# Kernel tuning notes

Hardware: AMD Instinct MI355X
Metric: run time of the kernel (lower is better)

The kernel has to match this reference:

```python
import jax, jax.numpy as jnp
import numpy as np

NEG_SLOPE = 0.2
# relation r: src node type SRC[r], dst node type DST[r]; 0=Drug, 1=Disease
# order: TREATS, TREATED_BY, HAS_CONTRAIND, CONTRAIND_BY, HAS_PARENTCODE, HAS_CHILDCODE, INTERACTS
SRC = (0, 1, 0, 1, 1, 1, 0)
DST = (1, 0, 1, 0, 1, 1, 0)

N_DRUG, N_DIS, D_IN, HID, OUT, E = 20000, 40000, 256, 128, 128, 150000


def _gat(x_src, x_dst, edge_index, Ws, Wd, a_s, a_d, b):
    # single-head PyG GATConv, add_self_loops=False
    hs = x_src @ Ws                      # [Ns, H]
    hd = x_dst @ Wd                      # [Nd, H]
    src, dst = edge_index[0], edge_index[1]
    n_dst = x_dst.shape[0]
    alpha_src = hs @ a_s                 # [Ns]
    alpha_dst = hd @ a_d                 # [Nd]
    alpha = jax.nn.leaky_relu(alpha_src[src] + alpha_dst[dst], NEG_SLOPE)  # [E]
    amax = jax.ops.segment_max(alpha, dst, num_segments=n_dst)
    amax = jnp.where(jnp.isfinite(amax), amax, 0.0)
    ex = jnp.exp(alpha - amax[dst])
    denom = jax.ops.segment_sum(ex, dst, num_segments=n_dst)
    coef = ex / (denom[dst] + 1e-16)     # per-destination softmax (PyG softmax)
    out = jax.ops.segment_sum(hs[src] * coef[:, None], dst, num_segments=n_dst)
    return out + b


def _hetero_layer(xd, xi, edges, Ws, Wd, a_s, a_d, b):
    feats = (xd, xi)
    H = b.shape[1]
    outs = [jnp.zeros((xd.shape[0], H), xd.dtype), jnp.zeros((xi.shape[0], H), xi.dtype)]
    for r in range(7):
        o = _gat(feats[SRC[r]], feats[DST[r]], edges[r], Ws[r], Wd[r], a_s[r], a_d[r], b[r])
        outs[DST[r]] = outs[DST[r]] + o   # HeteroConv aggr='sum'
    return outs[0], outs[1]


def setup_inputs() -> dict:
    key = jax.random.key(0)
    ks = jax.random.split(key, 32)
    x_drug = jax.random.normal(ks[0], (N_DRUG, D_IN), jnp.float32)
    x_disease = jax.random.normal(ks[1], (N_DIS, D_IN), jnp.float32)
    nsz = (N_DRUG, N_DIS)
    edges = []
    for r in range(7):
        s = jax.random.randint(ks[2 + 2 * r], (E,), 0, nsz[SRC[r]], jnp.int32)
        d = jax.random.randint(ks[3 + 2 * r], (E,), 0, nsz[DST[r]], jnp.int32)
        edges.append(jnp.stack([s, d]))
    s = 0.1
    W1s = s * jax.random.normal(ks[16], (7, D_IN, HID), jnp.float32)
    W1d = s * jax.random.normal(ks[17], (7, D_IN, HID), jnp.float32)
    W1d = W1d.at[6].set(W1s[6])  # INTERACTS shares src/dst lin (GATConv(-1,...))
    a1s = s * jax.random.normal(ks[18], (7, HID), jnp.float32)
    a1d = s * jax.random.normal(ks[19], (7, HID), jnp.float32)
    b1 = jnp.zeros((7, HID), jnp.float32)
    W2s = s * jax.random.normal(ks[20], (7, HID, HID), jnp.float32)
    W2d = s * jax.random.normal(ks[21], (7, HID, HID), jnp.float32)
    W2d = W2d.at[6].set(W2s[6])
    a2s = s * jax.random.normal(ks[22], (7, HID), jnp.float32)
    a2d = s * jax.random.normal(ks[23], (7, HID), jnp.float32)
    b2 = jnp.zeros((7, HID), jnp.float32)
    W_drug = s * jax.random.normal(ks[24], (HID, OUT), jnp.float32)
    b_drug = jnp.zeros((OUT,), jnp.float32)
    W_dis = s * jax.random.normal(ks[25], (HID, OUT), jnp.float32)
    b_dis = jnp.zeros((OUT,), jnp.float32)
    return {"x_drug": x_drug, "x_disease": x_disease,
            "e_treats": edges[0], "e_treated_by": edges[1], "e_contraind": edges[2],
            "e_contraind_by": edges[3], "e_parent": edges[4], "e_child": edges[5],
            "e_interacts": edges[6],
            "W1s": W1s, "W1d": W1d, "a1s": a1s, "a1d": a1d, "b1": b1,
            "W2s": W2s, "W2d": W2d, "a2s": a2s, "a2d": a2d, "b2": b2,
            "W_drug": W_drug, "b_drug": b_drug, "W_dis": W_dis, "b_dis": b_dis}


def reference(x_drug, x_disease, e_treats, e_treated_by, e_contraind, e_contraind_by,
              e_parent, e_child, e_interacts,
              W1s, W1d, a1s, a1d, b1, W2s, W2d, a2s, a2d, b2,
              W_drug, b_drug, W_dis, b_dis):
    edges = (e_treats, e_treated_by, e_contraind, e_contraind_by, e_parent, e_child, e_interacts)
    xd, xi = _hetero_layer(x_drug, x_disease, edges, W1s, W1d, a1s, a1d, b1)
    xd, xi = jax.nn.relu(xd), jax.nn.relu(xi)  # dropout is identity (eval mode)
    xd, xi = _hetero_layer(xd, xi, edges, W2s, W2d, a2s, a2d, b2)
    out_drug = jax.nn.relu(xd @ W_drug + b_drug)
    out_disease = jax.nn.relu(xi @ W_dis + b_dis)
    return out_drug, out_disease
```

## Files before the change

kernel.cpp:

```cpp
#include <hip/hip_runtime.h>
#include <stdint.h>

#define NDRUG 20000
#define NDIS  40000
#define HID   128
#define NE    150000
#define NREL  7
#define RPSTR (NDIS + 1)
#define NS_TOT (NREL * RPSTR)

typedef unsigned short ushort_t;
typedef __attribute__((ext_vector_type(8))) short bf16x8;
typedef __attribute__((ext_vector_type(4))) float f32x4;
typedef const __attribute__((address_space(1))) void gv_t;
typedef __attribute__((address_space(3))) void lv_t;

__device__ __forceinline__ ushort_t f2bf(float f) {
  unsigned u = __float_as_uint(f);
  u += 0x7FFFu + ((u >> 16) & 1u);
  return (ushort_t)(u >> 16);
}
__device__ __forceinline__ float bf2f(ushort_t h) {
  return __uint_as_float(((unsigned)h) << 16);
}

template<bool BIAS, bool RELU, bool BF16OUT>
__global__ __launch_bounds__(256) void mfma_gemm(
    const ushort_t* __restrict__ A, const ushort_t* __restrict__ BT,
    const float* __restrict__ bias, void* __restrict__ Cout, int M, int N, int K)
{
  __shared__ ushort_t As[128 * 32];
  __shared__ ushort_t Bs[128 * 32];
  const int tid = threadIdx.x;
  const int m0 = blockIdx.x * 128;
  const int n0 = blockIdx.y * 128;
  const int wave = tid >> 6, lane = tid & 63;
  const int wm = wave & 1, wn = wave >> 1;
  const int l15 = lane & 15, lk = lane >> 4;

  const int rowS = wave * 16 + (lane >> 2);
  const int chunk = (lane & 3) * 8;
  const int grA0 = min(m0 + rowS, M - 1);
  const int grA1 = min(m0 + rowS + 64, M - 1);
  const int grB0 = n0 + rowS;
  const int grB1 = n0 + rowS + 64;
  const ushort_t* ga0 = A + (size_t)grA0 * K + chunk;
  const ushort_t* ga1 = A + (size_t)grA1 * K + chunk;
  const ushort_t* gb0 = BT + (size_t)grB0 * K + chunk;
  const ushort_t* gb1 = BT + (size_t)grB1 * K + chunk;

  f32x4 acc[4][4] = {};

  for (int k0 = 0; k0 < K; k0 += 32) {
    __syncthreads();
    __builtin_amdgcn_global_load_lds((gv_t*)(ga0 + k0), (lv_t*)(As + wave * 512), 16, 0, 0);
    __builtin_amdgcn_global_load_lds((gv_t*)(ga1 + k0), (lv_t*)(As + wave * 512 + 2048), 16, 0, 0);
    __builtin_amdgcn_global_load_lds((gv_t*)(gb0 + k0), (lv_t*)(Bs + wave * 512), 16, 0, 0);
    __builtin_amdgcn_global_load_lds((gv_t*)(gb1 + k0), (lv_t*)(Bs + wave * 512 + 2048), 16, 0, 0);
    __syncthreads();

    bf16x8 af[4], bfg[4];
    #pragma unroll
    for (int m = 0; m < 4; ++m)
      af[m] = *reinterpret_cast<const bf16x8*>(&As[(wm * 64 + m * 16 + l15) * 32 + lk * 8]);
    #pragma unroll
    for (int n = 0; n < 4; ++n)
      bfg[n] = *reinterpret_cast<const bf16x8*>(&Bs[(wn * 64 + n * 16 + l15) * 32 + lk * 8]);
    #pragma unroll
    for (int m = 0; m < 4; ++m)
      #pragma unroll
      for (int n = 0; n < 4; ++n)
        acc[m][n] = __builtin_amdgcn_mfma_f32_16x16x32_bf16(af[m], bfg[n], acc[m][n], 0, 0, 0);
  }

  #pragma unroll
  for (int m = 0; m < 4; ++m) {
    int rbase = m0 + wm * 64 + m * 16 + lk * 4;
    #pragma unroll
    for (int n = 0; n < 4; ++n) {
      int col = n0 + wn * 64 + n * 16 + l15;
      float bv = 0.f;
      if (BIAS) bv = bias[col];
      #pragma unroll
      for (int j = 0; j < 4; ++j) {
        int row = rbase + j;
        if (row >= M) continue;
        float v = acc[m][n][j] + bv;
        if (RELU) v = fmaxf(v, 0.f);
        if (BF16OUT) ((ushort_t*)Cout)[(size_t)row * N + col] = f2bf(v);
        else         ((float*)Cout)[(size_t)row * N + col] = v;
      }
    }
  }
}

__global__ void build_wcatT(const float* __restrict__ W, ushort_t* __restrict__ out,
                            int K, int ncol, int4 rels)
{
  int id = blockIdx.x * 256 + threadIdx.x;
  int tot = K * ncol;
  if (id >= tot) return;
  int k = id / ncol, c = id - k * ncol;
  int rr = (&rels.x)[c >> 7];
  out[(size_t)c * K + k] = f2bf(W[((size_t)rr * K + k) * HID + (c & 127)]);
}

__global__ __launch_bounds__(256) void wvec_kernel(
    const float* __restrict__ Wsrc, const float* __restrict__ as_,
    const float* __restrict__ Wdst, const float* __restrict__ ad_,
    float* __restrict__ wv, int K)
{
  int slot = blockIdx.x;
  int r = slot % NREL;
  const float* W = (slot < NREL ? Wsrc : Wdst) + (size_t)r * K * HID;
  const float* a = (slot < NREL ? as_ : ad_) + r * HID;
  int wave = threadIdx.x >> 6, lane = threadIdx.x & 63;
  int k = blockIdx.y * 4 + wave;
  if (k >= K) return;
  float s = W[(size_t)k * HID + lane] * a[lane]
          + W[(size_t)k * HID + 64 + lane] * a[64 + lane];
  #pragma unroll
  for (int off = 32; off; off >>= 1) s += __shfl_xor(s, off);
  if (lane == 0) wv[slot * 256 + k] = s;
}

__global__ void cvt_f32_bf16(const float* __restrict__ in, ushort_t* __restrict__ out, int n8) {
  int i = blockIdx.x * 256 + threadIdx.x;
  if (i >= n8) return;
  float4 a = reinterpret_cast<const float4*>(in)[2 * i];
  float4 b = reinterpret_cast<const float4*>(in)[2 * i + 1];
  ushort_t r[8] = {f2bf(a.x), f2bf(a.y), f2bf(a.z), f2bf(a.w),
                   f2bf(b.x), f2bf(b.y), f2bf(b.z), f2bf(b.w)};
  reinterpret_cast<uint4*>(out)[i] = *reinterpret_cast<uint4*>(r);
}

struct AlphaJobs { int wslot[8]; int outOff[8]; };

template<int NV, int K>
__global__ __launch_bounds__(256) void alpha_batch(
    const ushort_t* __restrict__ X, int N, const float* __restrict__ wv,
    float* __restrict__ outBase, AlphaJobs jobs)
{
  int i = blockIdx.x * 256 + threadIdx.x;
  if (i >= N) return;
  float acc[NV];
  #pragma unroll
  for (int v = 0; v < NV; ++v) acc[v] = 0.f;
  const ushort_t* xp = X + (size_t)i * K;
  for (int k = 0; k < K; k += 8) {
    uint4 u = *reinterpret_cast<const uint4*>(xp + k);
    unsigned uu[4] = {u.x, u.y, u.z, u.w};
    float xf[8];
    #pragma unroll
    for (int q = 0; q < 4; ++q) {
      xf[2 * q]     = __uint_as_float(uu[q] << 16);
      xf[2 * q + 1] = __uint_as_float(uu[q] & 0xFFFF0000u);
    }
    #pragma unroll
    for (int v = 0; v < NV; ++v) {
      const float* wp = wv + jobs.wslot[v] * 256 + k;
      #pragma unroll
      for (int q = 0; q < 8; ++q) acc[v] += xf[q] * wp[q];
    }
  }
  #pragma unroll
  for (int v = 0; v < NV; ++v) outBase[jobs.outOff[v] + i] = acc[v];
}

struct RelIdx { const int* src[NREL]; const int* dst[NREL]; };
struct NdArr  { int nd[NREL]; };

__global__ void zero_ints(int* __restrict__ p, int n) {
  int i = blockIdx.x * 256 + threadIdx.x;
  if (i < n) p[i] = 0;
}
__global__ void hist_k(RelIdx ri, int* __restrict__ counts) {
  int e = blockIdx.x * 256 + threadIdx.x;
  int r = blockIdx.y;
  if (e >= NE) return;
  atomicAdd(&counts[r * RPSTR + ri.dst[r][e]], 1);
}
__global__ __launch_bounds__(256) void scan_blk(const int* __restrict__ in,
                                                int* __restrict__ partial,
                                                int* __restrict__ bsum, int n)
{
  __shared__ int ts[256];
  int t = threadIdx.x;
  int base = blockIdx.x * 1024 + t * 4;
  int v[4];
  #pragma unroll
  for (int i = 0; i < 4; ++i) v[i] = (base + i < n) ? in[base + i] : 0;
  int s = v[0] + v[1] + v[2] + v[3];
  ts[t] = s; __syncthreads();
  for (int off = 1; off < 256; off <<= 1) {
    int x = (t >= off) ? ts[t - off] : 0;
    __syncthreads();
    ts[t] += x;
    __syncthreads();
  }
  int run = ts[t] - s;
  #pragma unroll
  for (int i = 0; i < 4; ++i) {
    if (base + i < n) partial[base + i] = run;
    run += v[i];
  }
  if (t == 255) bsum[blockIdx.x] = ts[255];
}
__global__ __launch_bounds__(512) void scan_top(int* __restrict__ bsum, int nb) {
  __shared__ int ts[512];
  int t = threadIdx.x;
  int v = (t < nb) ? bsum[t] : 0;
  ts[t] = v; __syncthreads();
  for (int off = 1; off < 512; off <<= 1) {
    int x = (t >= off) ? ts[t - off] : 0;
    __syncthreads();
    ts[t] += x;
    __syncthreads();
  }
  if (t < nb) bsum[t] = ts[t] - v;
}
__global__ void scan_add(const int* __restrict__ partial, const int* __restrict__ bsum,
                         int* __restrict__ rowptr, int* __restrict__ cursor, int n)
{
  int i = blockIdx.x * 256 + threadIdx.x;
  if (i >= n) return;
  int v = partial[i] + bsum[i >> 10];
  rowptr[i] = v; cursor[i] = v;
}
__global__ void fill_k(RelIdx ri, int* __restrict__ cursor, int* __restrict__ colsrc) {
  int e = blockIdx.x * 256 + threadIdx.x;
  int r = blockIdx.y;
  if (e >= NE) return;
  int d = ri.dst[r][e];
  int pos = atomicAdd(&cursor[r * RPSTR + d], 1);
  colsrc[pos] = ri.src[r][e];
}

__global__ __launch_bounds__(256) void coef_k(
    const int* __restrict__ rowptr, const int* __restrict__ colsrc,
    const float* __restrict__ alphaB, float* __restrict__ coef, NdArr nds)
{
  int d = blockIdx.x * 256 + threadIdx.x;
  int r = blockIdx.y;
  if (d >= nds.nd[r]) return;
  int beg = rowptr[r * RPSTR + d], end = rowptr[r * RPSTR + d + 1];
  if (beg == end) return;
  const float ad = alphaB[(NREL + r) * NDIS + d];
  const float* as = alphaB + (size_t)r * NDIS;
  float m = -1e30f;
  for (int i = beg; i < end; ++i) {
    float a = as[colsrc[i]] + ad;
    a = a > 0.f ? a : 0.2f * a;
    m = fmaxf(m, a);
  }
  float sum = 0.f;
  for (int i = beg; i < end; ++i) {
    float a = as[colsrc[i]] + ad;
    a = a > 0.f ? a : 0.2f * a;
    float ex = __expf(a - m);
    coef[i] = ex;
    sum += ex;
  }
  float inv = 1.f / (sum + 1e-16f);
  for (int i = beg; i < end; ++i) coef[i] *= inv;
}

struct PvRel { int rel; int rowptr_off; const ushort_t* hs; int hst; int hoff; };
struct PvParams { PvRel dr[3]; PvRel di[4]; };

template<bool RELU>
__global__ __launch_bounds__(256) void pv_multi(
    PvParams P, const int* __restrict__ rowptr, const int* __restrict__ colsrc,
    const float* __restrict__ coef, const float* __restrict__ bias,
    ushort_t* __restrict__ outD, ushort_t* __restrict__ outI, int nbD)
{
  const int wave = threadIdx.x >> 6, lane = threadIdx.x & 63;
  const int c0 = lane * 2;
  const bool isD = blockIdx.x < (unsigned)nbD;
  const int d = (isD ? blockIdx.x : blockIdx.x - nbD) * 4 + wave;
  const int Nd = isD ? NDRUG : NDIS;
  if (d >= Nd) return;
  const int nr = isD ? 3 : 4;
  float acc0 = 0.f, acc1 = 0.f;

  for (int q = 0; q < nr; ++q) {
    const PvRel R = isD ? P.dr[q] : P.di[q];
    acc0 += bias[R.rel * HID + c0];
    acc1 += bias[R.rel * HID + c0 + 1];
    const int beg = rowptr[R.rowptr_off + d];
    const int end = rowptr[R.rowptr_off + d + 1];
    const ushort_t* hsb = R.hs + R.hoff + c0;
    const int hst = R.hst;
    for (int c = beg; c < end; c += 4) {
      float cf[4]; int si[4];
      #pragma unroll
      for (int j = 0; j < 4; ++j) {
        int idx = (c + j < end) ? c + j : end - 1;
        cf[j] = (c + j < end) ? coef[idx] : 0.f;
        si[j] = colsrc[idx];
      }
      ushort2 hv[4];
      #pragma unroll
      for (int j = 0; j < 4; ++j)
        hv[j] = *reinterpret_cast<const ushort2*>(hsb + (size_t)si[j] * hst);
      #pragma unroll
      for (int j = 0; j < 4; ++j) {
        acc0 += cf[j] * bf2f(hv[j].x);
        acc1 += cf[j] * bf2f(hv[j].y);
      }
    }
  }
  if (RELU) { acc0 = fmaxf(acc0, 0.f); acc1 = fmaxf(acc1, 0.f); }
  ushort_t* out = isD ? outD : outI;
  ushort2 o; o.x = f2bf(acc0); o.y = f2bf(acc1);
  *reinterpret_cast<ushort2*>(out + (size_t)d * HID + c0) = o;
}

struct WsPlan {
  ushort_t *xdb1, *xib1, *xd1b, *xi1b, *xd2b, *xi2b;
  ushort_t *hs_d, *hs_i, *wcatT_d, *wcatT_i, *wfinT_d, *wfinT_i;
  float *alphaB, *wv, *coef;
  int *counts, *rowptr, *cursor, *colsrc, *bsum;
  size_t total_bytes;
};

static WsPlan plan_ws(void* d_ws) {
  WsPlan p;
  ushort_t* s = (ushort_t*)d_ws;
  p.xdb1 = s;     s += (size_t)NDRUG * 256;
  p.xib1 = s;     s += (size_t)NDIS * 256;
  p.xd1b = s;     s += (size_t)NDRUG * HID;
  p.xi1b = s;     s += (size_t)NDIS * HID;
  p.hs_d = s;     s += (size_t)NDRUG * 384;
  p.hs_i = s;     s += (size_t)NDIS * 512;
  p.wcatT_d = s;  s += 384 * 256;
  p.wcatT_i = s;  s += 512 * 256;
  p.wfinT_d = s;  s += 128 * 128;
  p.wfinT_i = s;  s += 128 * 128;
  p.xd2b = p.xdb1;
  p.xi2b = p.xib1;
  float* f = (float*)s;
  p.alphaB = f;   f += (size_t)2 * NREL * NDIS;
  p.wv = f;       f += 14 * 256;
  p.coef = f;     f += (size_t)NREL * NE;
  int* q = (int*)f;
  p.counts = q;   q += NS_TOT;
  p.rowptr = q;   q += NS_TOT;
  p.cursor = q;   q += NS_TOT;
  p.colsrc = q;   q += NREL * NE;
  p.bsum = q;     q += 512;
  p.total_bytes = (size_t)((char*)q - (char*)d_ws);
  return p;
}

static void run_layer(const ushort_t* XDb, const ushort_t* XIb, int K,
                      const float* Wsrc, const float* Wdst,
                      const float* as_, const float* ad_, const float* bias,
                      ushort_t* outDb, ushort_t* outIb, bool relu,
                      const WsPlan& p, hipStream_t stream)
{
  int4 rd = make_int4(0, 2, 6, 0);
  int4 ri4 = make_int4(1, 3, 4, 5);
  build_wcatT<<<(K * 384 + 255) / 256, 256, 0, stream>>>(Wsrc, p.wcatT_d, K, 384, rd);
  build_wcatT<<<(K * 512 + 255) / 256, 256, 0, stream>>>(Wsrc, p.wcatT_i, K, 512, ri4);
  wvec_kernel<<<dim3(14, K / 4), 256, 0, stream>>>(Wsrc, as_, Wdst, ad_, p.wv, K);

  AlphaJobs jd = {};
  jd.wslot[0] = 0;     jd.outOff[0] = 0 * NDIS;
  jd.wslot[1] = 2;     jd.outOff[1] = 2 * NDIS;
  jd.wslot[2] = 6;     jd.outOff[2] = 6 * NDIS;
  jd.wslot[3] = 7 + 1; jd.outOff[3] = (7 + 1) * NDIS;
  jd.wslot[4] = 7 + 3; jd.outOff[4] = (7 + 3) * NDIS;
  jd.wslot[5] = 7 + 6; jd.outOff[5] = (7 + 6) * NDIS;
  AlphaJobs ji = {};
  ji.wslot[0] = 1;     ji.outOff[0] = 1 * NDIS;
  ji.wslot[1] = 3;     ji.outOff[1] = 3 * NDIS;
  ji.wslot[2] = 4;     ji.outOff[2] = 4 * NDIS;
  ji.wslot[3] = 5;     ji.outOff[3] = 5 * NDIS;
  ji.wslot[4] = 7 + 0; ji.outOff[4] = (7 + 0) * NDIS;
  ji.wslot[5] = 7 + 2; ji.outOff[5] = (7 + 2) * NDIS;
  ji.wslot[6] = 7 + 4; ji.outOff[6] = (7 + 4) * NDIS;
  ji.wslot[7] = 7 + 5; ji.outOff[7] = (7 + 5) * NDIS;
  int gbD = (NDRUG + 255) / 256, gbI = (NDIS + 255) / 256;
  if (K == 256) {
    alpha_batch<6, 256><<<gbD, 256, 0, stream>>>(XDb, NDRUG, p.wv, p.alphaB, jd);
    alpha_batch<8, 256><<<gbI, 256, 0, stream>>>(XIb, NDIS, p.wv, p.alphaB, ji);
  } else {
    alpha_batch<6, 128><<<gbD, 256, 0, stream>>>(XDb, NDRUG, p.wv, p.alphaB, jd);
    alpha_batch<8, 128><<<gbI, 256, 0, stream>>>(XIb, NDIS, p.wv, p.alphaB, ji);
  }

  mfma_gemm<false, false, true><<<dim3((NDRUG + 127) / 128, 3), 256, 0, stream>>>(
      XDb, p.wcatT_d, nullptr, p.hs_d, NDRUG, 384, K);
  mfma_gemm<false, false, true><<<dim3((NDIS + 127) / 128, 4), 256, 0, stream>>>(
      XIb, p.wcatT_i, nullptr, p.hs_i, NDIS, 512, K);

  NdArr nds;
  static const int DSTh[NREL] = {1, 0, 1, 0, 1, 1, 0};
  for (int r = 0; r < NREL; ++r) nds.nd[r] = DSTh[r] == 0 ? NDRUG : NDIS;
  coef_k<<<dim3((NDIS + 255) / 256, NREL), 256, 0, stream>>>(
      p.rowptr, p.colsrc, p.alphaB, p.coef, nds);

  PvParams P;
  P.dr[0] = {1, 1 * RPSTR, p.hs_i, 512, 0};
  P.dr[1] = {3, 3 * RPSTR, p.hs_i, 512, 128};
  P.dr[2] = {6, 6 * RPSTR, p.hs_d, 384, 256};
  P.di[0] = {0, 0 * RPSTR, p.hs_d, 384, 0};
  P.di[1] = {2, 2 * RPSTR, p.hs_d, 384, 128};
  P.di[2] = {4, 4 * RPSTR, p.hs_i, 512, 256};
  P.di[3] = {5, 5 * RPSTR, p.hs_i, 512, 384};
  int nbD = (NDRUG + 3) / 4, nbI = (NDIS + 3) / 4;
  if (relu)
    pv_multi<true><<<nbD + nbI, 256, 0, stream>>>(
        P, p.rowptr, p.colsrc, p.coef, bias, outDb, outIb, nbD);
  else
    pv_multi<false><<<nbD + nbI, 256, 0, stream>>>(
        P, p.rowptr, p.colsrc, p.coef, bias, outDb, outIb, nbD);
}

extern "C" void kernel_launch(void* const* d_in, const int* in_sizes, int n_in,
                              void* d_out, int out_size, void* d_ws, size_t ws_size,
                              hipStream_t stream) {
  const float* x_drug = (const float*)d_in[0];
  const float* x_dis  = (const float*)d_in[1];
  RelIdx ri;
  for (int r = 0; r < NREL; ++r) {
    const int* e = (const int*)d_in[2 + r];
    ri.src[r] = e; ri.dst[r] = e + NE;
  }
  const float* W1s = (const float*)d_in[9];
  const float* W1d = (const float*)d_in[10];
  const float* a1s = (const float*)d_in[11];
  const float* a1d = (const float*)d_in[12];
  const float* b1  = (const float*)d_in[13];
  const float* W2s = (const float*)d_in[14];
  const float* W2d = (const float*)d_in[15];
  const float* a2s = (const float*)d_in[16];
  const float* a2d = (const float*)d_in[17];
  const float* b2  = (const float*)d_in[18];
  const float* Wdr = (const float*)d_in[19];
  const float* bdr = (const float*)d_in[20];
  const float* Wdi = (const float*)d_in[21];
  const float* bdi = (const float*)d_in[22];

  WsPlan p = plan_ws(d_ws);
  if (p.total_bytes > ws_size) return;

  cvt_f32_bf16<<<(NDRUG * 256 / 8 + 255) / 256, 256, 0, stream>>>(x_drug, p.xdb1, NDRUG * 256 / 8);
  cvt_f32_bf16<<<(NDIS * 256 / 8 + 255) / 256, 256, 0, stream>>>(x_dis, p.xib1, NDIS * 256 / 8);

  zero_ints<<<(NS_TOT + 255) / 256, 256, 0, stream>>>(p.counts, NS_TOT);
  dim3 ge((NE + 255) / 256, NREL);
  hist_k<<<ge, 256, 0, stream>>>(ri, p.counts);
  int nb = (NS_TOT + 1023) / 1024;
  scan_blk<<<nb, 256, 0, stream>>>(p.counts, p.cursor, p.bsum, NS_TOT);
  scan_top<<<1, 512, 0, stream>>>(p.bsum, nb);
  scan_add<<<(NS_TOT + 255) / 256, 256, 0, stream>>>(p.cursor, p.bsum, p.rowptr, p.cursor, NS_TOT);
  fill_k<<<ge, 256, 0, stream>>>(ri, p.cursor, p.colsrc);

  run_layer(p.xdb1, p.xib1, 256, W1s, W1d, a1s, a1d, b1, p.xd1b, p.xi1b, true, p, stream);
  run_layer(p.xd1b, p.xi1b, 128, W2s, W2d, a2s, a2d, b2, p.xd2b, p.xi2b, false, p, stream);

  int4 r0 = make_int4(0, 0, 0, 0);
  build_wcatT<<<(128 * 128 + 255) / 256, 256, 0, stream>>>(Wdr, p.wfinT_d, 128, 128, r0);
  build_wcatT<<<(128 * 128 + 255) / 256, 256, 0, stream>>>(Wdi, p.wfinT_i, 128, 128, r0);
  float* out = (float*)d_out;
  mfma_gemm<true, true, false><<<dim3((NDRUG + 127) / 128, 1), 256, 0, stream>>>(
      p.xd2b, p.wfinT_d, bdr, out, NDRUG, 128, 128);
  mfma_gemm<true, true, false><<<dim3((NDIS + 127) / 128, 1), 256, 0, stream>>>(
      p.xi2b, p.wfinT_i, bdi, out + (size_t)NDRUG * HID, NDIS, 128, 128);
}
```

Measured before the change: 483.4 us.

## Merge paired launches, pack edge coef/src, defer softmax normalization, widen aggregation

Every pair of kernels that ran separately for drug and disease nodes (conversion, weight transpose, alpha, both GEMMs) now runs as one launch. Edge coefficients and source indices are stored interleaved as float2 so the aggregation kernel makes one gather per edge. The softmax normalization moves out of a separate pass into a per-destination inverse denominator applied after accumulation, and low-degree nodes keep their logits in registers instead of recomputing them. The aggregation kernel has each half-wave process alternating edges with 4 columns per lane, combined by a shuffle. This cuts launch count and memory passes, but the dual kernels add branching and the drug alpha path now computes two wasted dot products.

```diff
diff --git a/kernel.cpp b/kernel.cpp
--- a/kernel.cpp
+++ b/kernel.cpp
@@ -24,15 +24,19 @@
   return __uint_as_float(((unsigned)h) << 16);
 }
 
+struct GemmJob { const ushort_t* A; const ushort_t* BT; const float* bias; void* C; int M, N; };
+
 template<bool BIAS, bool RELU, bool BF16OUT>
-__global__ __launch_bounds__(256) void mfma_gemm(
-    const ushort_t* __restrict__ A, const ushort_t* __restrict__ BT,
-    const float* __restrict__ bias, void* __restrict__ Cout, int M, int N, int K)
+__global__ __launch_bounds__(256) void gemm_dual(GemmJob j0, GemmJob j1, int gx0, int K)
 {
   __shared__ ushort_t As[128 * 32];
   __shared__ ushort_t Bs[128 * 32];
+  const bool first = blockIdx.x < (unsigned)gx0;
+  const GemmJob J = first ? j0 : j1;
+  const int bx = first ? blockIdx.x : blockIdx.x - gx0;
+  if ((int)blockIdx.y * 128 >= J.N) return;
   const int tid = threadIdx.x;
-  const int m0 = blockIdx.x * 128;
+  const int m0 = bx * 128;
   const int n0 = blockIdx.y * 128;
   const int wave = tid >> 6, lane = tid & 63;
   const int wm = wave & 1, wn = wave >> 1;
@@ -40,14 +44,12 @@
 
   const int rowS = wave * 16 + (lane >> 2);
   const int chunk = (lane & 3) * 8;
-  const int grA0 = min(m0 + rowS, M - 1);
-  const int grA1 = min(m0 + rowS + 64, M - 1);
-  const int grB0 = n0 + rowS;
-  const int grB1 = n0 + rowS + 64;
-  const ushort_t* ga0 = A + (size_t)grA0 * K + chunk;
-  const ushort_t* ga1 = A + (size_t)grA1 * K + chunk;
-  const ushort_t* gb0 = BT + (size_t)grB0 * K + chunk;
-  const ushort_t* gb1 = BT + (size_t)grB1 * K + chunk;
+  const int grA0 = min(m0 + rowS, J.M - 1);
+  const int grA1 = min(m0 + rowS + 64, J.M - 1);
+  const ushort_t* ga0 = J.A + (size_t)grA0 * K + chunk;
+  const ushort_t* ga1 = J.A + (size_t)grA1 * K + chunk;
+  const ushort_t* gb0 = J.BT + (size_t)(n0 + rowS) * K + chunk;
+  const ushort_t* gb1 = J.BT + (size_t)(n0 + rowS + 64) * K + chunk;
 
   f32x4 acc[4][4] = {};
 
@@ -80,26 +82,34 @@
     for (int n = 0; n < 4; ++n) {
       int col = n0 + wn * 64 + n * 16 + l15;
       float bv = 0.f;
-      if (BIAS) bv = bias[col];
+      if (BIAS) bv = J.bias[col];
       #pragma unroll
       for (int j = 0; j < 4; ++j) {
         int row = rbase + j;
-        if (row >= M) continue;
+        if (row >= J.M) continue;
         float v = acc[m][n][j] + bv;
         if (RELU) v = fmaxf(v, 0.f);
-        if (BF16OUT) ((ushort_t*)Cout)[(size_t)row * N + col] = f2bf(v);
-        else         ((float*)Cout)[(size_t)row * N + col] = v;
+        if (BF16OUT) ((ushort_t*)J.C)[(size_t)row * J.N + col] = f2bf(v);
+        else         ((float*)J.C)[(size_t)row * J.N + col] = v;
       }
     }
   }
 }
 
-__global__ void build_wcatT(const float* __restrict__ W, ushort_t* __restrict__ out,
-                            int K, int ncol, int4 rels)
+__global__ void build_wcat2(const float* __restrict__ WA, ushort_t* __restrict__ outA,
+                            int ncolA, int4 relsA,
+                            const float* __restrict__ WB, ushort_t* __restrict__ outB,
+                            int ncolB, int4 relsB, int K)
 {
   int id = blockIdx.x * 256 + threadIdx.x;
-  int tot = K * ncol;
-  if (id >= tot) return;
+  const float* W; ushort_t* out; int ncol; int4 rels;
+  int totA = K * ncolA;
+  if (id < totA) { W = WA; out = outA; ncol = ncolA; rels = relsA; }
+  else {
+    id -= totA;
+    if (id >= K * ncolB) return;
+    W = WB; out = outB; ncol = ncolB; rels = relsB;
+  }
   int k = id / ncol, c = id - k * ncol;
   int rr = (&rels.x)[c >> 7];
   out[(size_t)c * K + k] = f2bf(W[((size_t)rr * K + k) * HID + (c & 127)]);
@@ -124,9 +134,17 @@
   if (lane == 0) wv[slot * 256 + k] = s;
 }
 
-__global__ void cvt_f32_bf16(const float* __restrict__ in, ushort_t* __restrict__ out, int n8) {
+__global__ void cvt2_f32_bf16(const float* __restrict__ inA, ushort_t* __restrict__ outA, int n8A,
+                              const float* __restrict__ inB, ushort_t* __restrict__ outB, int n8B)
+{
   int i = blockIdx.x * 256 + threadIdx.x;
-  if (i >= n8) return;
+  const float* in; ushort_t* out;
+  if (i < n8A) { in = inA; out = outA; }
+  else {
+    i -= n8A;
+    if (i >= n8B) return;
+    in = inB; out = outB;
+  }
   float4 a = reinterpret_cast<const float4*>(in)[2 * i];
   float4 b = reinterpret_cast<const float4*>(in)[2 * i + 1];
   ushort_t r[8] = {f2bf(a.x), f2bf(a.y), f2bf(a.z), f2bf(a.w),
@@ -136,16 +154,21 @@
 
 struct AlphaJobs { int wslot[8]; int outOff[8]; };
 
-template<int NV, int K>
-__global__ __launch_bounds__(256) void alpha_batch(
-    const ushort_t* __restrict__ X, int N, const float* __restrict__ wv,
-    float* __restrict__ outBase, AlphaJobs jobs)
-{
-  int i = blockIdx.x * 256 + threadIdx.x;
+template<int K>
+__global__ __launch_bounds__(256) void alpha_dual(
+    const ushort_t* __restrict__ XD, const ushort_t* __restrict__ XI,
+    const float* __restrict__ wv, float* __restrict__ outBase,
+    AlphaJobs jd, AlphaJobs ji, int gbD)
+{
+  const bool isD = blockIdx.x < (unsigned)gbD;
+  const ushort_t* X = isD ? XD : XI;
+  const int N = isD ? NDRUG : NDIS;
+  const AlphaJobs jobs = isD ? jd : ji;
+  int i = (isD ? blockIdx.x : blockIdx.x - gbD) * 256 + threadIdx.x;
   if (i >= N) return;
-  float acc[NV];
-  #pragma unroll
-  for (int v = 0; v < NV; ++v) acc[v] = 0.f;
+  float acc[8];
+  #pragma unroll
+  for (int v = 0; v < 8; ++v) acc[v] = 0.f;
   const ushort_t* xp = X + (size_t)i * K;
   for (int k = 0; k < K; k += 8) {
     uint4 u = *reinterpret_cast<const uint4*>(xp + k);
@@ -157,14 +180,14 @@
       xf[2 * q + 1] = __uint_as_float(uu[q] & 0xFFFF0000u);
     }
     #pragma unroll
-    for (int v = 0; v < NV; ++v) {
+    for (int v = 0; v < 8; ++v) {
       const float* wp = wv + jobs.wslot[v] * 256 + k;
       #pragma unroll
       for (int q = 0; q < 8; ++q) acc[v] += xf[q] * wp[q];
     }
   }
   #pragma unroll
-  for (int v = 0; v < NV; ++v) outBase[jobs.outOff[v] + i] = acc[v];
+  for (int v = 0; v < 8; ++v) outBase[jobs.outOff[v] + i] = acc[v];
 }
 
 struct RelIdx { const int* src[NREL]; const int* dst[NREL]; };
@@ -227,18 +250,18 @@
   int v = partial[i] + bsum[i >> 10];
   rowptr[i] = v; cursor[i] = v;
 }
-__global__ void fill_k(RelIdx ri, int* __restrict__ cursor, int* __restrict__ colsrc) {
+__global__ void fill_k(RelIdx ri, int* __restrict__ cursor, float2* __restrict__ pack) {
   int e = blockIdx.x * 256 + threadIdx.x;
   int r = blockIdx.y;
   if (e >= NE) return;
   int d = ri.dst[r][e];
   int pos = atomicAdd(&cursor[r * RPSTR + d], 1);
-  colsrc[pos] = ri.src[r][e];
+  ((int*)pack)[2 * (size_t)pos + 1] = ri.src[r][e];
 }
 
 __global__ __launch_bounds__(256) void coef_k(
-    const int* __restrict__ rowptr, const int* __restrict__ colsrc,
-    const float* __restrict__ alphaB, float* __restrict__ coef, NdArr nds)
+    const int* __restrict__ rowptr, float2* __restrict__ pack,
+    const float* __restrict__ alphaB, float* __restrict__ invden, NdArr nds)
 {
   int d = blockIdx.x * 256 + threadIdx.x;
   int r = blockIdx.y;
@@ -247,22 +270,48 @@
   if (beg == end) return;
   const float ad = alphaB[(NREL + r) * NDIS + d];
   const float* as = alphaB + (size_t)r * NDIS;
-  float m = -1e30f;
-  for (int i = beg; i < end; ++i) {
-    float a = as[colsrc[i]] + ad;
-    a = a > 0.f ? a : 0.2f * a;
-    m = fmaxf(m, a);
-  }
+  int deg = end - beg;
   float sum = 0.f;
-  for (int i = beg; i < end; ++i) {
-    float a = as[colsrc[i]] + ad;
-    a = a > 0.f ? a : 0.2f * a;
-    float ex = __expf(a - m);
-    coef[i] = ex;
-    sum += ex;
-  }
-  float inv = 1.f / (sum + 1e-16f);
-  for (int i = beg; i < end; ++i) coef[i] *= inv;
+  if (deg <= 16) {
+    float av[16];
+    float m = -1e30f;
+    #pragma unroll
+    for (int i = 0; i < 16; ++i) {
+      float a = -1e30f;
+      if (i < deg) {
+        int s = __float_as_int(pack[beg + i].y);
+        a = as[s] + ad;
+        a = a > 0.f ? a : 0.2f * a;
+      }
+      av[i] = a;
+      m = fmaxf(m, a);
+    }
+    #pragma unroll
+    for (int i = 0; i < 16; ++i) {
+      if (i < deg) {
+        float ex = __expf(av[i] - m);
+        ((float*)pack)[2 * (size_t)(beg + i)] = ex;
+        sum += ex;
+      }
+    }
+  } else {
+    float m = -1e30f;
+    for (int i = beg; i < end; ++i) {
+      int s = __float_as_int(pack[i].y);
+      float a = as[s] + ad;
+      a = a > 0.f ? a : 0.2f * a;
+      m = fmaxf(m, a);
+    }
+    for (int i = beg; i < end; ++i) {
+      int s = __float_as_int(pack[i].y);
+      float a = as[s] + ad;
+      a = a > 0.f ? a : 0.2f * a;
+      float ex = __expf(a - m);
+      ((float*)pack)[2 * (size_t)i] = ex;
+      sum += ex;
+    }
+  }
+  invden[r * NDIS + d] = 1.f / (sum + 1e-16f);
 }
 
 struct PvRel { int rel; int rowptr_off; const ushort_t* hs; int hst; int hoff; };
@@ -270,57 +319,82 @@
 
 template<bool RELU>
 __global__ __launch_bounds__(256) void pv_multi(
-    PvParams P, const int* __restrict__ rowptr, const int* __restrict__ colsrc,
-    const float* __restrict__ coef, const float* __restrict__ bias,
+    PvParams P, const int* __restrict__ rowptr, const float2* __restrict__ pack,
+    const float* __restrict__ invden, const float* __restrict__ bias,
     ushort_t* __restrict__ outD, ushort_t* __restrict__ outI, int nbD)
 {
   const int wave = threadIdx.x >> 6, lane = threadIdx.x & 63;
-  const int c0 = lane * 2;
+  const int half = lane >> 5, l31 = lane & 31;
+  const int c0 = l31 * 4;
   const bool isD = blockIdx.x < (unsigned)nbD;
   const int d = (isD ? blockIdx.x : blockIdx.x - nbD) * 4 + wave;
   const int Nd = isD ? NDRUG : NDIS;
   if (d >= Nd) return;
   const int nr = isD ? 3 : 4;
-  float acc0 = 0.f, acc1 = 0.f;
-
-  for (int q = 0; q < nr; ++q) {
+  float acc0 = 0.f, acc1 = 0.f, acc2 = 0.f, acc3 = 0.f;
+
+  #pragma unroll
+  for (int q = 0; q < 4; ++q) {
+    if (q >= nr) break;
     const PvRel R = isD ? P.dr[q] : P.di[q];
-    acc0 += bias[R.rel * HID + c0];
-    acc1 += bias[R.rel * HID + c0 + 1];
     const int beg = rowptr[R.rowptr_off + d];
     const int end = rowptr[R.rowptr_off + d + 1];
+    if (beg == end) continue;
     const ushort_t* hsb = R.hs + R.hoff + c0;
     const int hst = R.hst;
+    float p0 = 0.f, p1 = 0.f, p2 = 0.f, p3 = 0.f;
     for (int c = beg; c < end; c += 4) {
-      float cf[4]; int si[4];
-      #pragma unroll
-      for (int j = 0; j < 4; ++j) {
-        int idx = (c + j < end) ? c + j : end - 1;
-        cf[j] = (c + j < end) ? coef[idx] : 0.f;
-        si[j] = colsrc[idx];
-      }
-      ushort2 hv[4];
-      #pragma unroll
-      for (int j = 0; j < 4; ++j)
-        hv[j] = *reinterpret_cast<const ushort2*>(hsb + (size_t)si[j] * hst);
-      #pragma unroll
-      for (int j = 0; j < 4; ++j) {
-        acc0 += cf[j] * bf2f(hv[j].x);
-        acc1 += cf[j] * bf2f(hv[j].y);
-      }
-    }
-  }
-  if (RELU) { acc0 = fmaxf(acc0, 0.f); acc1 = fmaxf(acc1, 0.f); }
-  ushort_t* out = isD ? outD : outI;
-  ushort2 o; o.x = f2bf(acc0); o.y = f2bf(acc1);
-  *reinterpret_cast<ushort2*>(out + (size_t)d * HID + c0) = o;
-}
+      const int i0 = c + half, i1 = c + 2 + half;
+      const float2 e0 = pack[min(i0, end - 1)];
+      const float2 e1 = pack[min(i1, end - 1)];
+      const float cf0 = (i0 < end) ? e0.x : 0.f;
+      const float cf1 = (i1 < end) ? e1.x : 0.f;
+      const ushort4 h0 = *reinterpret_cast<const ushort4*>(
+          hsb + (size_t)__float_as_int(e0.y) * hst);
+      const ushort4 h1 = *reinterpret_cast<const ushort4*>(
+          hsb + (size_t)__float_as_int(e1.y) * hst);
+      p0 += cf0 * bf2f(h0.x); p1 += cf0 * bf2f(h0.y);
+      p2 += cf0 * bf2f(h0.z); p3 += cf0 * bf2f(h0.w);
+      p0 += cf1 * bf2f(h1.x); p1 += cf1 * bf2f(h1.y);
+      p2 += cf1 * bf2f(h1.z); p3 += cf1 * bf2f(h1.w);
+    }
+    const float inv = invden[R.rel * NDIS + d];
+    acc0 += p0 * inv; acc1 += p1 * inv; acc2 += p2 * inv; acc3 += p3 * inv;
+  }
+  acc0 += __shfl_xor(acc0, 32);
+  acc1 += __shfl_xor(acc1, 32);
+  acc2 += __shfl_xor(acc2, 32);
+  acc3 += __shfl_xor(acc3, 32);
+
+  if (half == 0) {
+    float b0 = 0.f, b1 = 0.f, b2 = 0.f, b3 = 0.f;
+    #pragma unroll
+    for (int q = 0; q < 4; ++q) {
+      if (q >= nr) break;
+      const PvRel R = isD ? P.dr[q] : P.di[q];
+      const float4 bv = *reinterpret_cast<const float4*>(&bias[R.rel * HID + c0]);
+      b0 += bv.x; b1 += bv.y; b2 += bv.z; b3 += bv.w;
+    }
+    acc0 += b0; acc1 += b1; acc2 += b2; acc3 += b3;
+    if (RELU) {
+      acc0 = fmaxf(acc0, 0.f); acc1 = fmaxf(acc1, 0.f);
+      acc2 = fmaxf(acc2, 0.f); acc3 = fmaxf(acc3, 0.f);
+    }
+    ushort_t* out = isD ? outD : outI;
+    ushort4 o;
+    o.x = f2bf(acc0); o.y = f2bf(acc1); o.z = f2bf(acc2); o.w = f2bf(acc3);
+    *reinterpret_cast<ushort4*>(out + (size_t)d * HID + c0) = o;
+  }
+}
+
+static const int DSTh[NREL] = {1, 0, 1, 0, 1, 1, 0};
 
 struct WsPlan {
   ushort_t *xdb1, *xib1, *xd1b, *xi1b, *xd2b, *xi2b;
   ushort_t *hs_d, *hs_i, *wcatT_d, *wcatT_i, *wfinT_d, *wfinT_i;
-  float *alphaB, *wv, *coef;
-  int *counts, *rowptr, *cursor, *colsrc, *bsum;
+  float2* pack;
+  float *alphaB, *wv, *invden;
+  int *counts, *rowptr, *cursor, *bsum;
   size_t total_bytes;
 };
 
@@ -339,15 +413,16 @@
   p.wfinT_i = s;  s += 128 * 128;
   p.xd2b = p.xdb1;
   p.xi2b = p.xib1;
-  float* f = (float*)s;
-  p.alphaB = f;   f += (size_t)2 * NREL * NDIS;
+  p.pack = (float2*)s;
+  float2* e = p.pack + (size_t)NREL * NE;
+  float* f = (float*)e;
+  p.alphaB = f;   f += (size_t)15 * NDIS;
   p.wv = f;       f += 14 * 256;
-  p.coef = f;     f += (size_t)NREL * NE;
+  p.invden = f;   f += (size_t)NREL * NDIS;
   int* q = (int*)f;
   p.counts = q;   q += NS_TOT;
   p.rowptr = q;   q += NS_TOT;
   p.cursor = q;   q += NS_TOT;
-  p.colsrc = q;   q += NREL * NE;
   p.bsum = q;     q += 512;
   p.total_bytes = (size_t)((char*)q - (char*)d_ws);
   return p;
@@ -361,8 +436,8 @@
 {
   int4 rd = make_int4(0, 2, 6, 0);
   int4 ri4 = make_int4(1, 3, 4, 5);
-  build_wcatT<<<(K * 384 + 255) / 256, 256, 0, stream>>>(Wsrc, p.wcatT_d, K, 384, rd);
-  build_wcatT<<<(K * 512 + 255) / 256, 256, 0, stream>>>(Wsrc, p.wcatT_i, K, 512, ri4);
+  build_wcat2<<<(K * 896 + 255) / 256, 256, 0, stream>>>(
+      Wsrc, p.wcatT_d, 384, rd, Wsrc, p.wcatT_i, 512, ri4, K);
   wvec_kernel<<<dim3(14, K / 4), 256, 0, stream>>>(Wsrc, as_, Wdst, ad_, p.wv, K);
 
   AlphaJobs jd = {};
@@ -372,6 +447,8 @@
   jd.wslot[3] = 7 + 1; jd.outOff[3] = (7 + 1) * NDIS;
   jd.wslot[4] = 7 + 3; jd.outOff[4] = (7 + 3) * NDIS;
   jd.wslot[5] = 7 + 6; jd.outOff[5] = (7 + 6) * NDIS;
+  jd.wslot[6] = 0;     jd.outOff[6] = 14 * NDIS;
+  jd.wslot[7] = 0;     jd.outOff[7] = 14 * NDIS;
   AlphaJobs ji = {};
   ji.wslot[0] = 1;     ji.outOff[0] = 1 * NDIS;
   ji.wslot[1] = 3;     ji.outOff[1] = 3 * NDIS;
@@ -382,24 +459,20 @@
   ji.wslot[6] = 7 + 4; ji.outOff[6] = (7 + 4) * NDIS;
   ji.wslot[7] = 7 + 5; ji.outOff[7] = (7 + 5) * NDIS;
   int gbD = (NDRUG + 255) / 256, gbI = (NDIS + 255) / 256;
-  if (K == 256) {
-    alpha_batch<6, 256><<<gbD, 256, 0, stream>>>(XDb, NDRUG, p.wv, p.alphaB, jd);
-    alpha_batch<8, 256><<<gbI, 256, 0, stream>>>(XIb, NDIS, p.wv, p.alphaB, ji);
-  } else {
-    alpha_batch<6, 128><<<gbD, 256, 0, stream>>>(XDb, NDRUG, p.wv, p.alphaB, jd);
-    alpha_batch<8, 128><<<gbI, 256, 0, stream>>>(XIb, NDIS, p.wv, p.alphaB, ji);
-  }
-
-  mfma_gemm<false, false, true><<<dim3((NDRUG + 127) / 128, 3), 256, 0, stream>>>(
-      XDb, p.wcatT_d, nullptr, p.hs_d, NDRUG, 384, K);
-  mfma_gemm<false, false, true><<<dim3((NDIS + 127) / 128, 4), 256, 0, stream>>>(
-      XIb, p.wcatT_i, nullptr, p.hs_i, NDIS, 512, K);
+  if (K == 256)
+    alpha_dual<256><<<gbD + gbI, 256, 0, stream>>>(XDb, XIb, p.wv, p.alphaB, jd, ji, gbD);
+  else
+    alpha_dual<128><<<gbD + gbI, 256, 0, stream>>>(XDb, XIb, p.wv, p.alphaB, jd, ji, gbD);
+
+  GemmJob g0 = {XDb, p.wcatT_d, nullptr, p.hs_d, NDRUG, 384};
+  GemmJob g1 = {XIb, p.wcatT_i, nullptr, p.hs_i, NDIS, 512};
+  int gx0 = (NDRUG + 127) / 128, gx1 = (NDIS + 127) / 128;
+  gemm_dual<false, false, true><<<dim3(gx0 + gx1, 4), 256, 0, stream>>>(g0, g1, gx0, K);
 
   NdArr nds;
-  static const int DSTh[NREL] = {1, 0, 1, 0, 1, 1, 0};
   for (int r = 0; r < NREL; ++r) nds.nd[r] = DSTh[r] == 0 ? NDRUG : NDIS;
   coef_k<<<dim3((NDIS + 255) / 256, NREL), 256, 0, stream>>>(
-      p.rowptr, p.colsrc, p.alphaB, p.coef, nds);
+      p.rowptr, p.pack, p.alphaB, p.invden, nds);
 
   PvParams P;
   P.dr[0] = {1, 1 * RPSTR, p.hs_i, 512, 0};
@@ -412,10 +485,10 @@
   int nbD = (NDRUG + 3) / 4, nbI = (NDIS + 3) / 4;
   if (relu)
     pv_multi<true><<<nbD + nbI, 256, 0, stream>>>(
-        P, p.rowptr, p.colsrc, p.coef, bias, outDb, outIb, nbD);
+        P, p.rowptr, p.pack, p.invden, bias, outDb, outIb, nbD);
   else
     pv_multi<false><<<nbD + nbI, 256, 0, stream>>>(
-        P, p.rowptr, p.colsrc, p.coef, bias, outDb, outIb, nbD);
+        P, p.rowptr, p.pack, p.invden, bias, outDb, outIb, nbD);
 }
 
 extern "C" void kernel_launch(void* const* d_in, const int* in_sizes, int n_in,
@@ -446,8 +519,8 @@
   WsPlan p = plan_ws(d_ws);
   if (p.total_bytes > ws_size) return;
 
-  cvt_f32_bf16<<<(NDRUG * 256 / 8 + 255) / 256, 256, 0, stream>>>(x_drug, p.xdb1, NDRUG * 256 / 8);
-  cvt_f32_bf16<<<(NDIS * 256 / 8 + 255) / 256, 256, 0, stream>>>(x_dis, p.xib1, NDIS * 256 / 8);
+  cvt2_f32_bf16<<<((NDRUG + NDIS) * 256 / 8 + 255) / 256, 256, 0, stream>>>(
+      x_drug, p.xdb1, NDRUG * 256 / 8, x_dis, p.xib1, NDIS * 256 / 8);
 
   zero_ints<<<(NS_TOT + 255) / 256, 256, 0, stream>>>(p.counts, NS_TOT);
   dim3 ge((NE + 255) / 256, NREL);
@@ -456,17 +529,17 @@
   scan_blk<<<nb, 256, 0, stream>>>(p.counts, p.cursor, p.bsum, NS_TOT);
   scan_top<<<1, 512, 0, stream>>>(p.bsum, nb);
   scan_add<<<(NS_TOT + 255) / 256, 256, 0, stream>>>(p.cursor, p.bsum, p.rowptr, p.cursor, NS_TOT);
-  fill_k<<<ge, 256, 0, stream>>>(ri, p.cursor, p.colsrc);
+  fill_k<<<ge, 256, 0, stream>>>(ri, p.cursor, p.pack);
 
   run_layer(p.xdb1, p.xib1, 256, W1s, W1d, a1s, a1d, b1, p.xd1b, p.xi1b, true, p, stream);
   run_layer(p.xd1b, p.xi1b, 128, W2s, W2d, a2s, a2d, b2, p.xd2b, p.xi2b, false, p, stream);
 
   int4 r0 = make_int4(0, 0, 0, 0);
-  build_wcatT<<<(128 * 128 + 255) / 256, 256, 0, stream>>>(Wdr, p.wfinT_d, 128, 128, r0);
-  build_wcatT<<<(128 * 128 + 255) / 256, 256, 0, stream>>>(Wdi, p.wfinT_i, 128, 128, r0);
+  build_wcat2<<<(128 * 128 * 2 + 255) / 256, 256, 0, stream>>>(
+      Wdr, p.wfinT_d, 128, r0, Wdi, p.wfinT_i, 128, r0, 128);
   float* out = (float*)d_out;
-  mfma_gemm<true, true, false><<<dim3((NDRUG + 127) / 128, 1), 256, 0, stream>>>(
-      p.xd2b, p.wfinT_d, bdr, out, NDRUG, 128, 128);
-  mfma_gemm<true, true, false><<<dim3((NDIS + 127) / 128, 1), 256, 0, stream>>>(
-      p.xi2b, p.wfinT_i, bdi, out + (size_t)NDRUG * HID, NDIS, 128, 128);
-}
+  GemmJob f0 = {p.xd2b, p.wfinT_d, bdr, out, NDRUG, 128};
+  GemmJob f1 = {p.xi2b, p.wfinT_i, bdi, out + (size_t)NDRUG * HID, NDIS, 128};
+  int gx0 = (NDRUG + 127) / 128, gx1 = (NDIS + 127) / 128;
+  gemm_dual<true, true, false><<<dim3(gx0 + gx1, 1), 256, 0, stream>>>(f0, f1, gx0, 128);
+}
```

Result: slower. 499.5 us (+3.3%).
